# Performance work log

Measured on AMD Instinct MI355X. Metric: run time of the kernel, lower is better.

## Reference

```python
import jax, jax.numpy as jnp
import numpy as np

B, N, E, K = 8, 4096, 1, 3
F = [16, 32, 16]
MLP_HID, MLP_OUT = 64, 1


def graph_filter(x, S, h, b):
    # x: [B, Fin, N], S: [E, N, N], h: [Fout, E, K, Fin], b: [Fout, 1]
    Bx, Fin, Nx = x.shape
    Ex, Kx = h.shape[1], h.shape[2]
    cur = jnp.broadcast_to(x[:, None], (Bx, Ex, Fin, Nx))  # tap 0: z = x
    zs = [cur]
    for _ in range(Kx - 1):
        cur = jnp.einsum('enm,befm->befn', S, cur)  # diffuse one hop
        zs.append(cur)
    z = jnp.stack(zs, axis=2)  # [B, E, K, Fin, N]
    return jnp.einsum('gekf,bekfn->bgn', h, z) + b[None]  # [B, Fout, N]


def gnn_layer(x, S, h, b, n_out):
    # GraphFilter -> ReLU -> NoPool (select first n_out nodes)
    return jax.nn.relu(graph_filter(x, S, h, b))[:, :, :n_out]


def setup_inputs() -> dict:
    key = jax.random.key(0)
    ks = jax.random.split(key, 16)
    sN = np.float32(1.0 / np.sqrt(N))
    x = jax.random.normal(ks[0], (B, F[0], N), dtype=jnp.float32)
    S_clique = jax.random.normal(ks[1], (E, N, N), dtype=jnp.float32) * sN
    S_line = jax.random.normal(ks[2], (E, N, N), dtype=jnp.float32) * sN

    def w(k, fo, fi):
        s = np.float32(1.0 / np.sqrt(fi * K))
        return jax.random.normal(k, (fo, E, K, fi), dtype=jnp.float32) * s

    Wc1, bc1 = w(ks[3], F[1], F[0]), jnp.zeros((F[1], 1), jnp.float32)
    Wc2, bc2 = w(ks[4], F[2], F[1]), jnp.zeros((F[2], 1), jnp.float32)
    Wl1, bl1 = w(ks[5], F[1], F[0]), jnp.zeros((F[1], 1), jnp.float32)
    Wl2, bl2 = w(ks[6], F[2], F[1]), jnp.zeros((F[2], 1), jnp.float32)
    d_in = N * F[-1]
    Wm1 = jax.random.normal(ks[7], (MLP_HID, d_in), dtype=jnp.float32) * np.float32(1.0 / np.sqrt(d_in))
    bm1 = jnp.zeros((MLP_HID,), jnp.float32)
    Wm2 = jax.random.normal(ks[8], (MLP_OUT, MLP_HID), dtype=jnp.float32) * np.float32(1.0 / np.sqrt(MLP_HID))
    bm2 = jnp.zeros((MLP_OUT,), jnp.float32)
    return {'x': x, 'S_clique': S_clique, 'S_line': S_line,
            'Wc1': Wc1, 'bc1': bc1, 'Wc2': Wc2, 'bc2': bc2,
            'Wl1': Wl1, 'bl1': bl1, 'Wl2': Wl2, 'bl2': bl2,
            'Wm1': Wm1, 'bm1': bm1, 'Wm2': Wm2, 'bm2': bm2}


def reference(x, S_clique, S_line, Wc1, bc1, Wc2, bc2, Wl1, bl1, Wl2, bl2, Wm1, bm1, Wm2, bm2):
    # clique-expansion branch (L=2 layers)
    y = gnn_layer(x, S_clique, Wc1, bc1, N)
    y = gnn_layer(y, S_clique, Wc2, bc2, N)
    # line-expansion branch (L=2 layers)
    y = gnn_layer(y, S_line, Wl1, bl1, N)
    y = gnn_layer(y, S_line, Wl2, bl2, N)
    yFlat = y.reshape(y.shape[0], -1)  # [B, F[-1]*N] (row-major matches torch)
    h = jax.nn.relu(yFlat @ Wm1.T + bm1)
    return h @ Wm2.T + bm2  # [B, 1]
```

## Files before the change

### kernel.cpp

```cpp
#include <hip/hip_runtime.h>


#define NN 4096
#define BB 8

typedef unsigned short u16;
typedef unsigned int   u32;

typedef __attribute__((ext_vector_type(8))) short bf16x8;
typedef __attribute__((ext_vector_type(4))) float f32x4;

__device__ __forceinline__ u16 f2bf(float f) {
    union { float f; u32 i; } c; c.f = f;
    u32 i = c.i;
    u32 r = (i + 0x7FFFu + ((i >> 16) & 1u)) >> 16;
    return (u16)r;
}
__device__ __forceinline__ float bf2f(u16 u) {
    union { u32 i; float f; } c; c.i = ((u32)u) << 16; return c.f;
}
__device__ __forceinline__ u32 pack2bf(float lo, float hi) {
    return (u32)f2bf(lo) | ((u32)f2bf(hi) << 16);
}

__device__ __forceinline__ void gload_lds16(const u16* g, u16* l) {
    __builtin_amdgcn_global_load_lds(
        (__attribute__((address_space(1))) void*)g,
        (__attribute__((address_space(3))) void*)l, 16, 0, 0);
}

__global__ __launch_bounds__(256) void cvt_x(const float* __restrict__ in,
                                             u16* __restrict__ out)
{
    const int i = (blockIdx.x * 256 + threadIdx.x) * 8;
    float4 a = *(const float4*)(in + i);
    float4 b = *(const float4*)(in + i + 4);
    uint4 o;
    o.x = pack2bf(a.x, a.y); o.y = pack2bf(a.z, a.w);
    o.z = pack2bf(b.x, b.y); o.w = pack2bf(b.z, b.w);
    *(uint4*)(out + i) = o;
}

template <int ITERS>
__global__ __launch_bounds__(256) void diffuse(const u16* __restrict__ Z,
                                               const u16* __restrict__ S,
                                               u16* __restrict__ Part)
{
    __shared__ u16 L[4 * 128 * 64];

    const int bx    = blockIdx.x;
    const int ntile = ((bx & 7) << 2) | (bx >> 3);
    const int nBase = ntile * 128;
    const int mBase = blockIdx.y * 128;
    const int tid   = threadIdx.x;
    const int lane  = tid & 63;
    const int wv    = tid >> 6;
    const int quad  = lane >> 4;
    const int l16   = lane & 15;
    const int wr    = (wv >> 1) * 64;
    const int wc    = (wv & 1) * 64;

    const int kStart = (int)blockIdx.z * (ITERS * 64);

    const int rl   = lane >> 3;
    const int gsl  = lane & 7;
    const int gsrc = gsl ^ rl;

    f32x4 acc[4][4];
#pragma unroll
    for (int i = 0; i < 4; ++i)
#pragma unroll
        for (int j = 0; j < 4; ++j) acc[i][j] = (f32x4){0.f, 0.f, 0.f, 0.f};

    auto stage = [&](int buf, int k0) {
#pragma unroll
        for (int j = 0; j < 4; ++j) {
            const int rb = wv * 32 + j * 8;
            gload_lds16(Z + (size_t)(mBase + rb + rl) * NN + k0 + gsrc * 8,
                        &L[buf * 8192 + rb * 64]);
            gload_lds16(S + (size_t)(nBase + rb + rl) * NN + k0 + gsrc * 8,
                        &L[16384 + buf * 8192 + rb * 64]);
        }
    };

    auto compute = [&](int buf) {
#pragma unroll
        for (int s = 0; s < 2; ++s) {
            const int g = s * 4 + quad;
            bf16x8 af[4], bf[4];
#pragma unroll
            for (int mi = 0; mi < 4; ++mi) {
                const int r = wr + mi * 16 + l16;
                af[mi] = *(const bf16x8*)&L[buf * 8192 + r * 64 + ((g ^ (r & 7)) << 3)];
            }
#pragma unroll
            for (int ni = 0; ni < 4; ++ni) {
                const int r = wc + ni * 16 + l16;
                bf[ni] = *(const bf16x8*)&L[16384 + buf * 8192 + r * 64 + ((g ^ (r & 7)) << 3)];
            }
#pragma unroll
            for (int mi = 0; mi < 4; ++mi)
#pragma unroll
                for (int ni = 0; ni < 4; ++ni)
                    acc[mi][ni] = __builtin_amdgcn_mfma_f32_16x16x32_bf16(
                        af[mi], bf[ni], acc[mi][ni], 0, 0, 0);
        }
    };

    stage(0, kStart);
#pragma unroll
    for (int i = 0; i < ITERS; ++i) {
        asm volatile("s_waitcnt vmcnt(0)" ::: "memory");
        __builtin_amdgcn_s_barrier();
        if (i + 1 < ITERS) stage((i + 1) & 1, kStart + (i + 1) * 64);
        compute(i & 1);
    }

    asm volatile("s_waitcnt lgkmcnt(0)" ::: "memory");
    __builtin_amdgcn_s_barrier();

    u16* tb = &L[wv * 4608];
#pragma unroll
    for (int mi = 0; mi < 4; ++mi)
#pragma unroll
        for (int ni = 0; ni < 4; ++ni)
#pragma unroll
            for (int i = 0; i < 4; ++i)
                tb[(mi * 16 + quad * 4 + i) * 72 + ni * 16 + l16] =
                    f2bf(acc[mi][ni][i]);

    const size_t plane = (size_t)gridDim.y * 128 * NN;
    u16* pp = Part + (size_t)blockIdx.z * plane;
    const int row0g = mBase + wr;
    const int col0g = nBase + wc;
#pragma unroll
    for (int j = 0; j < 8; ++j) {
        const int r = (lane >> 3) + j * 8;
        const int c = (lane & 7) * 8;
        bf16x8 v = *(const bf16x8*)&tb[r * 72 + c];
        *(bf16x8*)&pp[(size_t)(row0g + r) * NN + col0g + c] = v;
    }
}

template <int ITERS>
__global__ __launch_bounds__(256) void diffuse_cvtB(const u16* __restrict__ Z,
                                                    const float* __restrict__ Sf,
                                                    u16* __restrict__ Part,
                                                    u16* __restrict__ Sb)
{
    __shared__ u16 L[4 * 128 * 64];

    const int bx    = blockIdx.x;
    const int ntile = ((bx & 7) << 2) | (bx >> 3);
    const int nBase = ntile * 128;
    const int mBase = blockIdx.y * 128;
    const int tid   = threadIdx.x;
    const int lane  = tid & 63;
    const int wv    = tid >> 6;
    const int quad  = lane >> 4;
    const int l16   = lane & 15;
    const int wr    = (wv >> 1) * 64;
    const int wc    = (wv & 1) * 64;

    const int kStart = (int)blockIdx.z * (ITERS * 64);

    const int rl   = lane >> 3;
    const int gsl  = lane & 7;
    const int gsrc = gsl ^ rl;

    f32x4 acc[4][4];
#pragma unroll
    for (int i = 0; i < 4; ++i)
#pragma unroll
        for (int j = 0; j < 4; ++j) acc[i][j] = (f32x4){0.f, 0.f, 0.f, 0.f};

    auto stageA = [&](int buf, int k0) {
#pragma unroll
        for (int j = 0; j < 4; ++j) {
            const int rb = wv * 32 + j * 8;
            gload_lds16(Z + (size_t)(mBase + rb + rl) * NN + k0 + gsrc * 8,
                        &L[buf * 8192 + rb * 64]);
        }
    };

    float4 fB[4][2];
    auto loadB = [&](int k0) {
#pragma unroll
        for (int j = 0; j < 4; ++j) {
            const int row = nBase + wv * 32 + j * 8 + rl;
            const float* p = Sf + (size_t)row * NN + k0 + gsrc * 8;
            fB[j][0] = *(const float4*)p;
            fB[j][1] = *(const float4*)(p + 4);
        }
    };
    auto writeB = [&](int buf, int k0) {
#pragma unroll
        for (int j = 0; j < 4; ++j) {
            const int rloc = wv * 32 + j * 8 + rl;
            bf16x8 v;
            v[0] = (short)f2bf(fB[j][0].x); v[1] = (short)f2bf(fB[j][0].y);
            v[2] = (short)f2bf(fB[j][0].z); v[3] = (short)f2bf(fB[j][0].w);
            v[4] = (short)f2bf(fB[j][1].x); v[5] = (short)f2bf(fB[j][1].y);
            v[6] = (short)f2bf(fB[j][1].z); v[7] = (short)f2bf(fB[j][1].w);
            *(bf16x8*)&L[16384 + buf * 8192 + rloc * 64 + gsl * 8] = v;
            *(bf16x8*)&Sb[(size_t)(nBase + rloc) * NN + k0 + gsrc * 8] = v;
        }
    };

    auto compute = [&](int buf) {
#pragma unroll
        for (int s = 0; s < 2; ++s) {
            const int g = s * 4 + quad;
            bf16x8 af[4], bf[4];
#pragma unroll
            for (int mi = 0; mi < 4; ++mi) {
                const int r = wr + mi * 16 + l16;
                af[mi] = *(const bf16x8*)&L[buf * 8192 + r * 64 + ((g ^ (r & 7)) << 3)];
            }
#pragma unroll
            for (int ni = 0; ni < 4; ++ni) {
                const int r = wc + ni * 16 + l16;
                bf[ni] = *(const bf16x8*)&L[16384 + buf * 8192 + r * 64 + ((g ^ (r & 7)) << 3)];
            }
#pragma unroll
            for (int mi = 0; mi < 4; ++mi)
#pragma unroll
                for (int ni = 0; ni < 4; ++ni)
                    acc[mi][ni] = __builtin_amdgcn_mfma_f32_16x16x32_bf16(
                        af[mi], bf[ni], acc[mi][ni], 0, 0, 0);
        }
    };

    loadB(kStart);
    stageA(0, kStart);
    writeB(0, kStart);
    __syncthreads();

#pragma unroll
    for (int i = 0; i < ITERS; ++i) {
        const int k1 = kStart + (i + 1) * 64;
        if (i + 1 < ITERS) { stageA((i + 1) & 1, k1); loadB(k1); }
        compute(i & 1);
        if (i + 1 < ITERS) writeB((i + 1) & 1, k1);
        __syncthreads();
    }

    u16* tb = &L[wv * 4608];
#pragma unroll
    for (int mi = 0; mi < 4; ++mi)
#pragma unroll
        for (int ni = 0; ni < 4; ++ni)
#pragma unroll
            for (int i = 0; i < 4; ++i)
                tb[(mi * 16 + quad * 4 + i) * 72 + ni * 16 + l16] =
                    f2bf(acc[mi][ni][i]);

    const size_t plane = (size_t)gridDim.y * 128 * NN;
    u16* pp = Part + (size_t)blockIdx.z * plane;
    const int row0g = mBase + wr;
    const int col0g = nBase + wc;
#pragma unroll
    for (int j = 0; j < 8; ++j) {
        const int r = (lane >> 3) + j * 8;
        const int c = (lane & 7) * 8;
        bf16x8 v = *(const bf16x8*)&tb[r * 72 + c];
        *(bf16x8*)&pp[(size_t)(row0g + r) * NN + col0g + c] = v;
    }
}

template <int KS>
__global__ __launch_bounds__(256) void reduce_part(const u16* __restrict__ part,
                                                   int planeElems,
                                                   u16* __restrict__ outb)
{
    const int base   = (blockIdx.x * 256 + threadIdx.x) * 8;
    const int stride = gridDim.x * 256 * 8;
    for (int i = base; i < planeElems; i += stride) {
        float s[8];
#pragma unroll
        for (int e = 0; e < 8; ++e) s[e] = 0.f;
#pragma unroll
        for (int p = 0; p < KS; ++p) {
            uint4 v = *(const uint4*)(part + (size_t)p * planeElems + i);
            const u32 w[4] = {v.x, v.y, v.z, v.w};
#pragma unroll
            for (int q = 0; q < 4; ++q) {
                union { u32 i; float f; } lo, hi;
                lo.i = w[q] << 16;
                hi.i = w[q] & 0xFFFF0000u;
                s[q * 2]     += lo.f;
                s[q * 2 + 1] += hi.f;
            }
        }
        uint4 o;
        o.x = (u32)f2bf(s[0]) | ((u32)f2bf(s[1]) << 16);
        o.y = (u32)f2bf(s[2]) | ((u32)f2bf(s[3]) << 16);
        o.z = (u32)f2bf(s[4]) | ((u32)f2bf(s[5]) << 16);
        o.w = (u32)f2bf(s[6]) | ((u32)f2bf(s[7]) << 16);
        *(uint4*)(outb + i) = o;
    }
}

template <int FIN, int FOUT, int KS>
__global__ __launch_bounds__(256) void combine_relu(
    const u16* __restrict__ z0, const u16* __restrict__ z1,
    const u16* __restrict__ part2, int planeElems,
    const float* __restrict__ W, const float* __restrict__ bias,
    u16* __restrict__ out)
{
    __shared__ float hs[FOUT * 3 * FIN];
    __shared__ float bs[FOUT];
    for (int i = threadIdx.x; i < FOUT * 3 * FIN; i += 256) hs[i] = W[i];
    if (threadIdx.x < FOUT) bs[threadIdx.x] = bias[threadIdx.x];
    __syncthreads();

    const int nb = NN / 256;
    const int b  = blockIdx.x / nb;
    const int n  = (blockIdx.x % nb) * 256 + threadIdx.x;

    float zv[3][FIN];
    const u16* zp0 = z0 + (size_t)b * FIN * NN + n;
    const u16* zp1 = z1 + (size_t)b * FIN * NN + n;
    const u16* zp2 = part2 + (size_t)b * FIN * NN + n;
#pragma unroll
    for (int f = 0; f < FIN; ++f) {
        zv[0][f] = bf2f(zp0[(size_t)f * NN]);
        zv[1][f] = bf2f(zp1[(size_t)f * NN]);
        float s = 0.f;
#pragma unroll
        for (int p = 0; p < KS; ++p)
            s += bf2f(zp2[(size_t)p * planeElems + (size_t)f * NN]);
        zv[2][f] = s;
    }

    u16* op = out + (size_t)b * FOUT * NN + n;
    for (int g = 0; g < FOUT; ++g) {
        float acc = bs[g];
#pragma unroll
        for (int k = 0; k < 3; ++k)
#pragma unroll
            for (int f = 0; f < FIN; ++f)
                acc = fmaf(hs[(g * 3 + k) * FIN + f], zv[k][f], acc);
        op[(size_t)g * NN] = f2bf(fmaxf(acc, 0.f));
    }
}

__global__ __launch_bounds__(256) void mlp1(const u16* __restrict__ y,
                                            const float* __restrict__ Wm1,
                                            float* __restrict__ h1p)
{
    const int j    = blockIdx.x;
    const int base = blockIdx.y * 8192;
    const int D    = 16 * NN;

    float acc[BB];
#pragma unroll
    for (int b = 0; b < BB; ++b) acc[b] = 0.f;

    const float* wrow = Wm1 + (size_t)j * D + base;
    for (int idx = threadIdx.x * 8; idx < 8192; idx += 256 * 8) {
        float4 w0 = *(const float4*)(wrow + idx);
        float4 w1 = *(const float4*)(wrow + idx + 4);
#pragma unroll
        for (int b = 0; b < BB; ++b) {
            uint4 yv = *(const uint4*)(y + (size_t)b * D + base + idx);
            union { u32 i; float f; } c[8];
            c[0].i = yv.x << 16; c[1].i = yv.x & 0xFFFF0000u;
            c[2].i = yv.y << 16; c[3].i = yv.y & 0xFFFF0000u;
            c[4].i = yv.z << 16; c[5].i = yv.z & 0xFFFF0000u;
            c[6].i = yv.w << 16; c[7].i = yv.w & 0xFFFF0000u;
            acc[b] = fmaf(w0.x, c[0].f, acc[b]);
            acc[b] = fmaf(w0.y, c[1].f, acc[b]);
            acc[b] = fmaf(w0.z, c[2].f, acc[b]);
            acc[b] = fmaf(w0.w, c[3].f, acc[b]);
            acc[b] = fmaf(w1.x, c[4].f, acc[b]);
            acc[b] = fmaf(w1.y, c[5].f, acc[b]);
            acc[b] = fmaf(w1.z, c[6].f, acc[b]);
            acc[b] = fmaf(w1.w, c[7].f, acc[b]);
        }
    }

    __shared__ float red[BB][4];
    const int lane = threadIdx.x & 63;
    const int w    = threadIdx.x >> 6;
#pragma unroll
    for (int b = 0; b < BB; ++b) {
        float v = acc[b];
        for (int off = 32; off > 0; off >>= 1) v += __shfl_down(v, off, 64);
        if (lane == 0) red[b][w] = v;
    }
    __syncthreads();
    if (threadIdx.x < BB) {
        const int b = threadIdx.x;
        h1p[blockIdx.y * (BB * 64) + b * 64 + j] =
            red[b][0] + red[b][1] + red[b][2] + red[b][3];
    }
}

__global__ void mlp2(const float* __restrict__ h1p,
                     const float* __restrict__ bm1,
                     const float* __restrict__ Wm2,
                     const float* __restrict__ bm2, float* __restrict__ out)
{
    const int lane = threadIdx.x;
    const float w    = Wm2[lane];
    const float b1   = bm1[lane];
    const float bias = bm2[0];
    for (int b = 0; b < BB; ++b) {
        float h = 0.f;
#pragma unroll
        for (int p = 0; p < 8; ++p) h += h1p[p * (BB * 64) + b * 64 + lane];
        float v = fmaxf(h + b1, 0.f) * w;
        for (int off = 32; off > 0; off >>= 1) v += __shfl_down(v, off, 64);
        if (lane == 0) out[b] = v + bias;
    }
}

extern "C" void kernel_launch(void* const* d_in, const int* in_sizes, int n_in,
                              void* d_out, int out_size, void* d_ws, size_t ws_size,
                              hipStream_t stream)
{
    const float* x   = (const float*)d_in[0];
    const float* Sc  = (const float*)d_in[1];
    const float* Sl  = (const float*)d_in[2];
    const float* Wc1 = (const float*)d_in[3];
    const float* bc1 = (const float*)d_in[4];
    const float* Wc2 = (const float*)d_in[5];
    const float* bc2 = (const float*)d_in[6];
    const float* Wl1 = (const float*)d_in[7];
    const float* bl1 = (const float*)d_in[8];
    const float* Wl2 = (const float*)d_in[9];
    const float* bl2 = (const float*)d_in[10];
    const float* Wm1 = (const float*)d_in[11];
    const float* bm1 = (const float*)d_in[12];
    const float* Wm2 = (const float*)d_in[13];
    const float* bm2 = (const float*)d_in[14];
    float* out = (float*)d_out;

    char* ws = (char*)d_ws;
    u16*   part = (u16*)(ws);
    u16*   zb1  = (u16*)(ws + (16u << 20));
    u16*   yPa  = (u16*)(ws + (18u << 20));
    u16*   yPb  = (u16*)(ws + (20u << 20));
    float* h1p  = (float*)(ws + (22u << 20));
    u16*   Sb   = (u16*)(ws + (23u << 20));

    const dim3 blk(256);
    const dim3 gridCmb(BB * NN / 256);
    const dim3 g128(32, 1, 16);
    const dim3 g256(32, 2, 8);
    const int  pl128 = 128 * NN;
    const int  pl256 = 256 * NN;

    cvt_x<<<256, blk, 0, stream>>>(x, yPa);

    diffuse_cvtB<4><<<g128, blk, 0, stream>>>(yPa, Sc, part, Sb);
    reduce_part<16><<<256, blk, 0, stream>>>(part, pl128, zb1);
    diffuse<4><<<g128, blk, 0, stream>>>(zb1, Sb, part);
    combine_relu<16, 32, 16><<<gridCmb, blk, 0, stream>>>(yPa, zb1, part, pl128,
                                                          Wc1, bc1, yPb);
    diffuse<8><<<g256, blk, 0, stream>>>(yPb, Sb, part);
    reduce_part<8><<<512, blk, 0, stream>>>(part, pl256, zb1);
    diffuse<8><<<g256, blk, 0, stream>>>(zb1, Sb, part);
    combine_relu<32, 16, 8><<<gridCmb, blk, 0, stream>>>(yPb, zb1, part, pl256,
                                                         Wc2, bc2, yPa);
    diffuse_cvtB<4><<<g128, blk, 0, stream>>>(yPa, Sl, part, Sb);
    reduce_part<16><<<256, blk, 0, stream>>>(part, pl128, zb1);
    diffuse<4><<<g128, blk, 0, stream>>>(zb1, Sb, part);
    combine_relu<16, 32, 16><<<gridCmb, blk, 0, stream>>>(yPa, zb1, part, pl128,
                                                          Wl1, bl1, yPb);
    diffuse<8><<<g256, blk, 0, stream>>>(yPb, Sb, part);
    reduce_part<8><<<512, blk, 0, stream>>>(part, pl256, zb1);
    diffuse<8><<<g256, blk, 0, stream>>>(zb1, Sb, part);
    combine_relu<32, 16, 8><<<gridCmb, blk, 0, stream>>>(yPb, zb1, part, pl256,
                                                         Wl2, bl2, yPa);
    mlp1<<<dim3(64, 8), blk, 0, stream>>>(yPa, Wm1, h1p);
    mlp2<<<1, 64, 0, stream>>>(h1p, bm1, Wm2, bm2, out);
}
```

Baseline: 400.8 us.

## Triple-buffer diffuse loads and halve split-K partitions

The diffuse kernel moves from a double-buffered to a triple-buffered LDS pipeline, issuing global-to-LDS loads two stages ahead and waiting with partial vmcnt, plus an extra barrier per iteration. The split-K factor is halved (ITERS doubled), which reduces partial-sum traffic and reduce work but leaves fewer blocks in flight. The clique and line bf16 S matrices now get separate workspace buffers, and the workspace layout is compacted. Larger LDS use (96KB) may lower occupancy.

```diff
diff --git a/kernel.cpp b/kernel.cpp
--- a/kernel.cpp
+++ b/kernel.cpp
@@ -46,7 +46,7 @@
                                                const u16* __restrict__ S,
                                                u16* __restrict__ Part)
 {
-    __shared__ u16 L[4 * 128 * 64];
+    __shared__ u16 L[6 * 8192];
 
     const int bx    = blockIdx.x;
     const int ntile = ((bx & 7) << 2) | (bx >> 3);
@@ -79,7 +79,7 @@
             gload_lds16(Z + (size_t)(mBase + rb + rl) * NN + k0 + gsrc * 8,
                         &L[buf * 8192 + rb * 64]);
             gload_lds16(S + (size_t)(nBase + rb + rl) * NN + k0 + gsrc * 8,
-                        &L[16384 + buf * 8192 + rb * 64]);
+                        &L[24576 + buf * 8192 + rb * 64]);
         }
     };
 
@@ -96,7 +96,7 @@
 #pragma unroll
             for (int ni = 0; ni < 4; ++ni) {
                 const int r = wc + ni * 16 + l16;
-                bf[ni] = *(const bf16x8*)&L[16384 + buf * 8192 + r * 64 + ((g ^ (r & 7)) << 3)];
+                bf[ni] = *(const bf16x8*)&L[24576 + buf * 8192 + r * 64 + ((g ^ (r & 7)) << 3)];
             }
 #pragma unroll
             for (int mi = 0; mi < 4; ++mi)
@@ -108,12 +108,20 @@
     };
 
     stage(0, kStart);
+    stage(1, kStart + 64);
+
 #pragma unroll
     for (int i = 0; i < ITERS; ++i) {
-        asm volatile("s_waitcnt vmcnt(0)" ::: "memory");
+        if (i + 2 < ITERS) stage((i + 2) % 3, kStart + (i + 2) * 64);
+        if (i < ITERS - 2)
+            asm volatile("s_waitcnt vmcnt(16)" ::: "memory");
+        else if (i == ITERS - 2)
+            asm volatile("s_waitcnt vmcnt(8)" ::: "memory");
+        else
+            asm volatile("s_waitcnt vmcnt(0)" ::: "memory");
         __builtin_amdgcn_s_barrier();
-        if (i + 1 < ITERS) stage((i + 1) & 1, kStart + (i + 1) * 64);
-        compute(i & 1);
+        compute(i % 3);
+        if (i + 1 < ITERS) __builtin_amdgcn_s_barrier();
     }
 
     asm volatile("s_waitcnt lgkmcnt(0)" ::: "memory");
@@ -148,7 +156,7 @@
                                                     u16* __restrict__ Part,
                                                     u16* __restrict__ Sb)
 {
-    __shared__ u16 L[4 * 128 * 64];
+    __shared__ u16 L[4 * 8192];
 
     const int bx    = blockIdx.x;
     const int ntile = ((bx & 7) << 2) | (bx >> 3);
@@ -439,40 +447,41 @@
 
     char* ws = (char*)d_ws;
     u16*   part = (u16*)(ws);
-    u16*   zb1  = (u16*)(ws + (16u << 20));
-    u16*   yPa  = (u16*)(ws + (18u << 20));
-    u16*   yPb  = (u16*)(ws + (20u << 20));
-    float* h1p  = (float*)(ws + (22u << 20));
-    u16*   Sb   = (u16*)(ws + (23u << 20));
+    u16*   zb1  = (u16*)(ws + (8u  << 20));
+    u16*   yPa  = (u16*)(ws + (12u << 20));
+    u16*   yPb  = (u16*)(ws + (14u << 20));
+    float* h1p  = (float*)(ws + (16u << 20));
+    u16*   Scb  = (u16*)(ws + (17u << 20));
+    u16*   Slb  = Scb + (size_t)NN * NN;
 
     const dim3 blk(256);
     const dim3 gridCmb(BB * NN / 256);
-    const dim3 g128(32, 1, 16);
-    const dim3 g256(32, 2, 8);
+    const dim3 g128(32, 1, 8);
+    const dim3 g256(32, 2, 4);
     const int  pl128 = 128 * NN;
     const int  pl256 = 256 * NN;
 
     cvt_x<<<256, blk, 0, stream>>>(x, yPa);
 
-    diffuse_cvtB<4><<<g128, blk, 0, stream>>>(yPa, Sc, part, Sb);
-    reduce_part<16><<<256, blk, 0, stream>>>(part, pl128, zb1);
-    diffuse<4><<<g128, blk, 0, stream>>>(zb1, Sb, part);
-    combine_relu<16, 32, 16><<<gridCmb, blk, 0, stream>>>(yPa, zb1, part, pl128,
-                                                          Wc1, bc1, yPb);
-    diffuse<8><<<g256, blk, 0, stream>>>(yPb, Sb, part);
-    reduce_part<8><<<512, blk, 0, stream>>>(part, pl256, zb1);
-    diffuse<8><<<g256, blk, 0, stream>>>(zb1, Sb, part);
-    combine_relu<32, 16, 8><<<gridCmb, blk, 0, stream>>>(yPb, zb1, part, pl256,
+    diffuse_cvtB<8><<<g128, blk, 0, stream>>>(yPa, Sc, part, Scb);
+    reduce_part<8><<<256, blk, 0, stream>>>(part, pl128, zb1);
+    diffuse<8><<<g128, blk, 0, stream>>>(zb1, Scb, part);
+    combine_relu<16, 32, 8><<<gridCmb, blk, 0, stream>>>(yPa, zb1, part, pl128,
+                                                         Wc1, bc1, yPb);
+    diffuse<16><<<g256, blk, 0, stream>>>(yPb, Scb, part);
+    reduce_part<4><<<512, blk, 0, stream>>>(part, pl256, zb1);
+    diffuse<16><<<g256, blk, 0, stream>>>(zb1, Scb, part);
+    combine_relu<32, 16, 4><<<gridCmb, blk, 0, stream>>>(yPb, zb1, part, pl256,
                                                          Wc2, bc2, yPa);
-    diffuse_cvtB<4><<<g128, blk, 0, stream>>>(yPa, Sl, part, Sb);
-    reduce_part<16><<<256, blk, 0, stream>>>(part, pl128, zb1);
-    diffuse<4><<<g128, blk, 0, stream>>>(zb1, Sb, part);
-    combine_relu<16, 32, 16><<<gridCmb, blk, 0, stream>>>(yPa, zb1, part, pl128,
-                                                          Wl1, bl1, yPb);
-    diffuse<8><<<g256, blk, 0, stream>>>(yPb, Sb, part);
-    reduce_part<8><<<512, blk, 0, stream>>>(part, pl256, zb1);
-    diffuse<8><<<g256, blk, 0, stream>>>(zb1, Sb, part);
-    combine_relu<32, 16, 8><<<gridCmb, blk, 0, stream>>>(yPb, zb1, part, pl256,
+    diffuse_cvtB<8><<<g128, blk, 0, stream>>>(yPa, Sl, part, Slb);
+    reduce_part<8><<<256, blk, 0, stream>>>(part, pl128, zb1);
+    diffuse<8><<<g128, blk, 0, stream>>>(zb1, Slb, part);
+    combine_relu<16, 32, 8><<<gridCmb, blk, 0, stream>>>(yPa, zb1, part, pl128,
+                                                         Wl1, bl1, yPb);
+    diffuse<16><<<g256, blk, 0, stream>>>(yPb, Slb, part);
+    reduce_part<4><<<512, blk, 0, stream>>>(part, pl256, zb1);
+    diffuse<16><<<g256, blk, 0, stream>>>(zb1, Slb, part);
+    combine_relu<32, 16, 4><<<gridCmb, blk, 0, stream>>>(yPb, zb1, part, pl256,
                                                          Wl2, bl2, yPa);
     mlp1<<<dim3(64, 8), blk, 0, stream>>>(yPa, Wm1, h1p);
     mlp2<<<1, 64, 0, stream>>>(h1p, bm1, Wm2, bm2, out);
```

After: 367.3 us, median of 2. -8.4%, faster.
